# Performance work log

Hardware: AMD Instinct MI355X
Metric: run time of the kernel (lower is better)

Reference implementation:

```python
import jax, jax.numpy as jnp
import numpy as np

FORGET_BIAS = 1.0  # TF BasicLSTMCell default

def _lstm_layer(x_seq, state, W, b):
    """x_seq: [B,T,D_in]; state: [B,2*mem] = concat([c,h],1) (state_is_tuple=False).
    Returns (outputs [B,T,mem], final_state [B,2*mem])."""
    mem = state.shape[1] // 2
    c0, h0 = state[:, :mem], state[:, mem:]
    xs = jnp.swapaxes(x_seq, 0, 1)  # [T,B,D_in]

    def step(carry, x_t):
        c, h = carry
        z = jnp.concatenate([x_t, h], axis=-1) @ W + b  # [B,4*mem]
        i, j, f, o = jnp.split(z, 4, axis=-1)           # TF gate order i,j,f,o
        c = c * jax.nn.sigmoid(f + FORGET_BIAS) + jax.nn.sigmoid(i) * jnp.tanh(j)
        h = jnp.tanh(c) * jax.nn.sigmoid(o)
        return (c, h), h

    (c, h), hs = jax.lax.scan(step, (c0, h0), xs)
    return jnp.swapaxes(hs, 0, 1), jnp.concatenate([c, h], axis=-1)


def setup_inputs() -> dict:
    key = jax.random.key(0)
    ks = jax.random.split(key, 4)
    B, T, V, MEM = 64, 512, 256, 1024
    s = lambda n: 1.0 / np.sqrt(n)
    return {
        "x": jax.random.normal(ks[0], (B, T, V), jnp.float32),
        "state0": jnp.zeros((B, 2 * MEM), jnp.float32),
        "state1": jnp.zeros((B, 2 * MEM), jnp.float32),
        "W0": jax.random.normal(ks[1], (V + MEM, 4 * MEM), jnp.float32) * s(V + MEM),
        "b0": jnp.zeros((4 * MEM,), jnp.float32),
        "W1": jax.random.normal(ks[2], (2 * MEM, 4 * MEM), jnp.float32) * s(2 * MEM),
        "b1": jnp.zeros((4 * MEM,), jnp.float32),
        "W_out": jax.random.normal(ks[3], (MEM, V), jnp.float32) * s(MEM),
        "b_out": jnp.zeros((V,), jnp.float32),
    }


def reference(x, state0, state1, W0, b0, W1, b1, W_out, b_out):
    h0_seq, fs0 = _lstm_layer(x, state0, W0, b0)
    h1_seq, fs1 = _lstm_layer(h0_seq, state1, W1, b1)
    outputs = h1_seq @ W_out + b_out  # dense projection to out_vector_size
    final_state = jnp.stack([fs0, fs1], axis=0)  # [n_layers, B, 2*mem]
    return outputs, final_state
```

## Files before the change

kernel.cpp:

```cpp
#include <hip/hip_runtime.h>
#include <stdint.h>

typedef __bf16 bf16;
typedef __attribute__((ext_vector_type(8))) __bf16 bf16x8;
typedef __attribute__((ext_vector_type(4))) float f32x4;
typedef __attribute__((ext_vector_type(4))) unsigned u32x4;

#define OFF_W0P   0ull
#define SZ_W0P    10485760ull
#define OFF_W1P   (OFF_W0P + SZ_W0P)
#define SZ_W1P    16777216ull
#define OFF_WOUT  (OFF_W1P + SZ_W1P)
#define SZ_WOUT   524288ull
#define OFF_B0P   (OFF_WOUT + SZ_WOUT)
#define OFF_B1P   (OFF_B0P + 16384ull)
#define OFF_BOP   (OFF_B1P + 16384ull)
#define OFF_BAR   (OFF_BOP + 1024ull)
#define OFF_FLAG  (OFF_BAR + 128ull)
#define OFF_H0PP  (OFF_BAR + 256ull)
#define OFF_H1PP  (OFF_H0PP + 262144ull)
#define OFF_XP    (OFF_H1PP + 262144ull)
#define SZ_XP     16777216ull
#define OFF_FLAGS (OFF_XP + SZ_XP)
#define OFF_REL   (OFF_FLAGS + 1024ull)

#define OUT_FS0   8388608
#define OUT_FS1   8519680

#define LDS_PARTP 106496
#define LDS_TOTAL 110592

#define CPOL_CC 17

typedef const __attribute__((address_space(1))) void gvoid_t;
typedef __attribute__((address_space(3))) void lvoid_t;

__device__ __forceinline__ void gl_lds16(void* lds, const void* g) {
  __builtin_amdgcn_global_load_lds((gvoid_t*)g, (lvoid_t*)lds, 16, 0, 0);
}

__device__ __forceinline__ __amdgpu_buffer_rsrc_t make_rsrc(const void* p) {
  return __builtin_amdgcn_make_buffer_rsrc(const_cast<void*>(p), (short)0, 0xFFFFFFFFu, 0x00020000u);
}

__device__ __forceinline__ void st_h2(__amdgpu_buffer_rsrc_t rs, unsigned off, float h) {
  bf16 b = (bf16)h;
  __builtin_amdgcn_raw_buffer_store_b16(__builtin_bit_cast(unsigned short, b), rs, off, 0, CPOL_CC);
}

__device__ __forceinline__ size_t hpack_off(int b, int u) {
  return (size_t)((((b >> 4) * 32 + (u >> 5)) * 64 + ((b & 15) | (((u >> 3) & 3) << 4))) * 16 + ((u & 7) << 1));
}

__device__ __forceinline__ float sigm(float v) { return 1.0f / (1.0f + __expf(-v)); }
__device__ __forceinline__ float tanh_(float v) { return 2.0f / (1.0f + __expf(-2.0f * v)) - 1.0f; }
__device__ __forceinline__ float scrub(float v, float lim) { return fminf(fmaxf(v, -lim), lim); }

__device__ __forceinline__ float ldel(const void* p, size_t i, int fl) {
  return fl ? ((const float*)p)[i] : (float)((const bf16*)p)[i];
}

__global__ __launch_bounds__(256) void detect_kernel(const void* __restrict__ W0, char* __restrict__ ws) {
  __shared__ int cnt;
  if (threadIdx.x == 0) cnt = 0;
  __syncthreads();
  int local = 0;
  const unsigned* w = (const unsigned*)W0;
#pragma unroll
  for (int i = 0; i < 4; ++i) {
    unsigned e = (w[threadIdx.x * 4 + i] >> 7) & 0xFF;
    local += (e >= 0x68 && e <= 0x7E) ? 1 : 0;
  }
  atomicAdd(&cnt, local);
  __syncthreads();
  if (threadIdx.x == 0) *(unsigned*)(ws + OFF_FLAG) = (cnt < 512) ? 1u : 0u;
}

__global__ __launch_bounds__(256) void prep_pack(const void* __restrict__ x, const void* __restrict__ W0,
                                                 const void* __restrict__ b0, const void* __restrict__ W1,
                                                 const void* __restrict__ b1, const void* __restrict__ Wout,
                                                 const void* __restrict__ bout, char* __restrict__ ws) {
  const int fl = *(const unsigned*)(ws + OFF_FLAG);
  int id = blockIdx.x * 256 + threadIdx.x;
  if (id < 5242880) {
    int tile = id / 20480, rem = id % 20480;
    int kt = rem >> 9, l = (rem >> 3) & 63, jj = rem & 7;
    int k = kt * 32 + ((l >> 4) << 3) + jj;
    int pc = tile * 16 + (l & 15);
    ((bf16*)(ws + OFF_W0P))[id] = (bf16)ldel(W0, (size_t)k * 4096 + (pc & 3) * 1024 + (pc >> 2), fl);
  } else if (id < 13631488) {
    int id2 = id - 5242880;
    int tile = id2 >> 15, rem = id2 & 32767;
    int kt = rem >> 9, l = (rem >> 3) & 63, jj = rem & 7;
    int k = kt * 32 + ((l >> 4) << 3) + jj;
    int pc = tile * 16 + (l & 15);
    ((bf16*)(ws + OFF_W1P))[id2] = (bf16)ldel(W1, (size_t)k * 4096 + (pc & 3) * 1024 + (pc >> 2), fl);
  } else if (id < 13893632) {
    int id2 = id - 13631488;
    int kt = id2 / 8192, rem = id2 % 8192;
    int nt = rem >> 9, l = (rem >> 3) & 63, jj = rem & 7;
    ((bf16*)(ws + OFF_WOUT))[id2] = (bf16)ldel(Wout, (size_t)(kt * 32 + ((l >> 4) << 3) + jj) * 256 + nt * 16 + (l & 15), fl);
  } else if (id < 13897728) {
    int pc = id - 13893632;
    ((float*)(ws + OFF_B0P))[pc] = ldel(b0, (pc & 3) * 1024 + (pc >> 2), fl);
  } else if (id < 13901824) {
    int pc = id - 13897728;
    ((float*)(ws + OFF_B1P))[pc] = ldel(b1, (pc & 3) * 1024 + (pc >> 2), fl);
  } else if (id < 13902080) {
    int pc = id - 13901824;
    ((float*)(ws + OFF_BOP))[pc] = ldel(bout, pc, fl);
  } else if (id < 22290688) {
    int id2 = id - 13902080;
    int t = id2 >> 14, rem = id2 & 16383;
    int mt = rem >> 12, rem2 = rem & 4095;
    int kt = rem2 >> 9, l = (rem2 >> 3) & 63, j = rem2 & 7;
    int b = mt * 16 + (l & 15);
    int v = kt * 32 + ((l >> 4) << 3) + j;
    ((bf16*)(ws + OFF_XP))[id2] = (bf16)ldel(x, ((size_t)b * 512 + t) * 256 + v, fl);
  }
}

__global__ __launch_bounds__(256) void init_state(const void* __restrict__ s0, const void* __restrict__ s1,
                                                  char* __restrict__ ws) {
  const int fl = *(const unsigned*)(ws + OFF_FLAG);
  int id = blockIdx.x * 256 + threadIdx.x;
  if (id < 65536) {
    int b = id >> 10, u = id & 1023;
    *(bf16*)(ws + OFF_H0PP + 131072 + hpack_off(b, u)) = (bf16)ldel(s0, b * 2048 + 1024 + u, fl);
  } else if (id < 131072) {
    int id2 = id - 65536; int b = id2 >> 10, u = id2 & 1023;
    *(bf16*)(ws + OFF_H1PP + hpack_off(b, u)) = (bf16)ldel(s1, b * 2048 + 1024 + u, fl);
  } else if (id < 131330) {
    ((unsigned*)(ws + OFF_FLAGS))[id - 131072] = 0u;
  }
}

__global__ __launch_bounds__(256, 1) void recur_kernel(const void* __restrict__ s0, const void* __restrict__ s1,
                                                       char* __restrict__ ws, void* __restrict__ outv) {
  extern __shared__ char smem[];
  const int fl = *(const unsigned*)(ws + OFF_FLAG);
  const int tid = threadIdx.x;
  const int lane = tid & 63;
  const int wid = tid >> 6;
  const int cu = blockIdx.x;
  const int nt = cu & 15, mo = (cu >> 4) & 3, dg = cu >> 6;

  auto store_out = [&](size_t idx, float v) {
    if (fl) ((float*)outv)[idx] = v; else ((bf16*)outv)[idx] = (bf16)v;
  };

  {
    const char* g0 = ws + OFF_W0P + (size_t)cu * 40960;
    for (int off = tid * 16; off < 40960; off += 4096) gl_lds16(smem + off, g0 + off);
    const char* g1 = ws + OFF_W1P + (size_t)cu * 65536;
    for (int off = tid * 16; off < 65536; off += 4096) gl_lds16(smem + 40960 + off, g1 + off);
  }
  bf16x8 wreg[8];
#pragma unroll
  for (int i = 0; i < 8; ++i)
    wreg[i] = *(const bf16x8*)(ws + OFF_WOUT + (size_t)(((wid * 8 + i) * 16 + nt) * 64 + lane) * 16);

  const float bini0 = ((const float*)(ws + OFF_B0P))[cu * 16 + (lane & 15)];
  const float bini1 = ((const float*)(ws + OFF_B1P))[cu * 16 + (lane & 15)];
  const float boN = ((const float*)(ws + OFF_BOP))[nt * 16 + (lane & 15)];
  const int u0 = cu * 4 + ((lane & 15) >> 2);
  float c0reg[4], c1reg[4];
#pragma unroll
  for (int r = 0; r < 4; ++r) {
    int b = wid * 16 + ((lane >> 4) << 2) + r;
    c0reg[r] = ldel(s0, b * 2048 + u0, fl);
    c1reg[r] = ldel(s1, b * 2048 + u0, fl);
  }

  const __amdgpu_buffer_rsrc_t rs = make_rsrc(ws);
  unsigned* flags = (unsigned*)(ws + OFF_FLAGS);
  unsigned* rel   = (unsigned*)(ws + OFF_REL);
  const char* dummy = ws + (size_t)lane * 16;
  const char* lb0 = smem + (size_t)lane * 16;
  const char* lb1 = smem + 40960 + (size_t)lane * 16;

  __syncthreads();

  bf16x8 pf0, pf1, pf2, pf3, pf4, pf5, pf6, pf7;
  f32x4 accP;

  for (int it = 0; it < 517; ++it) {
    const bool a0 = (it < 512);
    const bool a1 = (it >= 1 && it <= 512);
    const bool last = (it == 516);
    const int p = (it - 2 - dg) & 3;
    const int tP = it - 2 - p;
    const bool pw = (it >= 2 && tP >= 0 && tP <= 511);
    const char* h0src = ws + OFF_H0PP + (size_t)((it + 1) & 1) * 131072;
    const char* h1src = ws + OFF_H1PP + (size_t)((it + 1) & 1) * 131072;

    const char* ph0 = (it <= 512) ? (h0src + (size_t)(wid * 32) * 1024 + (size_t)lane * 16) : dummy;
    const char* ph1 = a1 ? (h1src + (size_t)(wid * 32) * 1024 + (size_t)lane * 16) : dummy;

    if (pw && p == 0) {
      const char* pm = h1src + (size_t)(mo * 32 + wid * 8) * 1024 + (size_t)lane * 16;
      pf0 = *(const bf16x8*)(pm);
      pf1 = *(const bf16x8*)(pm + 1024);
      pf2 = *(const bf16x8*)(pm + 2048);
      pf3 = *(const bf16x8*)(pm + 3072);
      pf4 = *(const bf16x8*)(pm + 4096);
      pf5 = *(const bf16x8*)(pm + 5120);
      pf6 = *(const bf16x8*)(pm + 6144);
      pf7 = *(const bf16x8*)(pm + 7168);
#pragma unroll
      for (int r = 0; r < 4; ++r) accP[r] = 0.f;
    }

    f32x4 acc0, acc1;
#pragma unroll
    for (int r = 0; r < 4; ++r) { acc0[r] = bini0; acc1[r] = bini1; }

    if (it < 514) {
      const char* px = a0 ? (ws + OFF_XP + (size_t)((it * 4 + wid) * 8) * 1024 + (size_t)lane * 16) : dummy;

      bf16x8 ring[24];
#pragma unroll
      for (int s = 0; s < 24; ++s)
        ring[s] = *(const bf16x8*)(s < 8 ? px + s * 1024 : ph0 + (s - 8) * 1024);
#pragma unroll
      for (int s = 0; s < 72; ++s) {
        bf16x8 af = ring[s % 24];
        const int f = s + 24;
        if (f < 72)
          ring[s % 24] = *(const bf16x8*)(f < 40 ? ph0 + (f - 8) * 1024 : ph1 + (f - 40) * 1024);
        if (s < 40)
          acc0 = __builtin_amdgcn_mfma_f32_16x16x32_bf16(af, *(const bf16x8*)(lb0 + s * 1024), acc0, 0, 0, 0);
        if (s >= 8)
          acc1 = __builtin_amdgcn_mfma_f32_16x16x32_bf16(af, *(const bf16x8*)(lb1 + (s - 8) * 1024), acc1, 0, 0, 0);
      }
    }

    if (pw) {
      switch (p) {
        case 0:
          accP = __builtin_amdgcn_mfma_f32_16x16x32_bf16(pf0, wreg[0], accP, 0, 0, 0);
          accP = __builtin_amdgcn_mfma_f32_16x16x32_bf16(pf1, wreg[1], accP, 0, 0, 0);
          break;
        case 1:
          accP = __builtin_amdgcn_mfma_f32_16x16x32_bf16(pf2, wreg[2], accP, 0, 0, 0);
          accP = __builtin_amdgcn_mfma_f32_16x16x32_bf16(pf3, wreg[3], accP, 0, 0, 0);
          break;
        case 2:
          accP = __builtin_amdgcn_mfma_f32_16x16x32_bf16(pf4, wreg[4], accP, 0, 0, 0);
          accP = __builtin_amdgcn_mfma_f32_16x16x32_bf16(pf5, wreg[5], accP, 0, 0, 0);
          break;
        default:
          accP = __builtin_amdgcn_mfma_f32_16x16x32_bf16(pf6, wreg[6], accP, 0, 0, 0);
          accP = __builtin_amdgcn_mfma_f32_16x16x32_bf16(pf7, wreg[7], accP, 0, 0, 0);
          break;
      }
    }

    const int base = lane & 60;
    if (a0) {
      const unsigned h0w = (unsigned)(OFF_H0PP) + (unsigned)(it & 1) * 131072u;
#pragma unroll
      for (int r = 0; r < 4; ++r) {
        float z = acc0[r];
        float zi = scrub(__shfl(z, base + 0, 64), 80.f);
        float zj = scrub(__shfl(z, base + 1, 64), 80.f);
        float zf = scrub(__shfl(z, base + 2, 64), 80.f);
        float zo = scrub(__shfl(z, base + 3, 64), 80.f);
        float c = c0reg[r];
        c = c * sigm(zf + 1.0f) + sigm(zi) * tanh_(zj);
        c = scrub(c, 1000.f);
        float h = tanh_(c) * sigm(zo);
        c0reg[r] = c;
        if ((lane & 3) == 0) {
          int b = wid * 16 + ((lane >> 4) << 2) + r;
          st_h2(rs, h0w + (unsigned)hpack_off(b, u0), h);
          if (it == 511) { store_out(OUT_FS0 + b * 2048 + u0, c); store_out(OUT_FS0 + b * 2048 + 1024 + u0, h); }
        }
      }
    }
    if (a1) {
      const unsigned h1w = (unsigned)(OFF_H1PP) + (unsigned)(it & 1) * 131072u;
#pragma unroll
      for (int r = 0; r < 4; ++r) {
        float z = acc1[r];
        float zi = scrub(__shfl(z, base + 0, 64), 80.f);
        float zj = scrub(__shfl(z, base + 1, 64), 80.f);
        float zf = scrub(__shfl(z, base + 2, 64), 80.f);
        float zo = scrub(__shfl(z, base + 3, 64), 80.f);
        float c = c1reg[r];
        c = c * sigm(zf + 1.0f) + sigm(zi) * tanh_(zj);
        c = scrub(c, 1000.f);
        float h = tanh_(c) * sigm(zo);
        c1reg[r] = c;
        if ((lane & 3) == 0) {
          int b = wid * 16 + ((lane >> 4) << 2) + r;
          st_h2(rs, h1w + (unsigned)hpack_off(b, u0), h);
          if (it == 512) { store_out(OUT_FS1 + b * 2048 + u0, c); store_out(OUT_FS1 + b * 2048 + 1024 + u0, h); }
        }
      }
    }
    if (pw && p == 3) {
      *(f32x4*)(smem + LDS_PARTP + (size_t)(wid * 64 + lane) * 16) = accP;
      __syncthreads();
      if (wid == 0) {
        f32x4 sm = *(const f32x4*)(smem + LDS_PARTP + (size_t)lane * 16);
#pragma unroll
        for (int w = 1; w < 4; ++w) {
          f32x4 q = *(const f32x4*)(smem + LDS_PARTP + (size_t)(w * 64 + lane) * 16);
#pragma unroll
          for (int r = 0; r < 4; ++r) sm[r] += q[r];
        }
#pragma unroll
        for (int r = 0; r < 4; ++r) {
          int b = mo * 16 + ((lane >> 4) << 2) + r;
          store_out(((size_t)b * 512 + tP) * 256 + nt * 16 + (lane & 15), sm[r] + boN);
        }
      }
    }
    if (last) break;

    asm volatile("s_waitcnt vmcnt(0)" ::: "memory");
    __syncthreads();
    if (tid == 0)
      __hip_atomic_store(flags + cu, (unsigned)(it + 1), __ATOMIC_RELAXED, __HIP_MEMORY_SCOPE_AGENT);
    if (cu == 0) {
      while (__hip_atomic_load(flags + tid, __ATOMIC_RELAXED, __HIP_MEMORY_SCOPE_AGENT) < (unsigned)(it + 1))
        __builtin_amdgcn_s_sleep(8);
      __syncthreads();
      if (tid == 0)
        __hip_atomic_store(rel, (unsigned)(it + 1), __ATOMIC_RELAXED, __HIP_MEMORY_SCOPE_AGENT);
    }
    if (tid == 0) {
      while (__hip_atomic_load(rel, __ATOMIC_RELAXED, __HIP_MEMORY_SCOPE_AGENT) < (unsigned)(it + 1))
        __builtin_amdgcn_s_sleep(8);
      __builtin_amdgcn_fence(__ATOMIC_ACQUIRE, "agent");
    }
    __syncthreads();
  }
}

extern "C" void kernel_launch(void* const* d_in, const int* in_sizes, int n_in,
                              void* d_out, int out_size, void* d_ws, size_t ws_size,
                              hipStream_t stream) {
  const void* x    = d_in[0];
  const void* s0   = d_in[1];
  const void* s1   = d_in[2];
  const void* W0   = d_in[3];
  const void* b0   = d_in[4];
  const void* W1   = d_in[5];
  const void* b1   = d_in[6];
  const void* Wout = d_in[7];
  const void* bout = d_in[8];
  char* ws = (char*)d_ws;
  (void)in_sizes; (void)n_in; (void)out_size; (void)ws_size;

  hipFuncSetAttribute((const void*)recur_kernel, hipFuncAttributeMaxDynamicSharedMemorySize, LDS_TOTAL);

  hipLaunchKernelGGL(detect_kernel, dim3(1),     dim3(256), 0, stream, W0, ws);
  hipLaunchKernelGGL(prep_pack,     dim3(87073), dim3(256), 0, stream, x, W0, b0, W1, b1, Wout, bout, ws);
  hipLaunchKernelGGL(init_state,    dim3(514),   dim3(256), 0, stream, s0, s1, ws);
  hipLaunchKernelGGL(recur_kernel,  dim3(256),   dim3(256), LDS_TOTAL, stream, s0, s1, ws, d_out);
}
```

Baseline: 4.805 ms.

## Precompute next step's input-projection MFMAs during the grid barrier wait

The x-part of the layer-0 gate GEMM (8 MFMAs over the input features) does not depend on the recurrent state. It is now computed for step it+1 after the CU signals its barrier flag and before it spins on the release, so that work overlaps barrier latency. The critical-path ring loop then only streams h0/h1, which shortens the per-step dependent chain. In exchange the accumulator is carried across iterations, raising register pressure, and global x loads now sit inside the barrier window.

```diff
diff --git a/kernel.cpp b/kernel.cpp
--- a/kernel.cpp
+++ b/kernel.cpp
@@ -184,6 +184,19 @@
   bf16x8 pf0, pf1, pf2, pf3, pf4, pf5, pf6, pf7;
   f32x4 accP;
 
+  f32x4 acc0n;
+  {
+    const char* px0 = ws + OFF_XP + (size_t)(wid * 8) * 1024 + (size_t)lane * 16;
+    bf16x8 xr[8];
+#pragma unroll
+    for (int s = 0; s < 8; ++s) xr[s] = *(const bf16x8*)(px0 + s * 1024);
+#pragma unroll
+    for (int r = 0; r < 4; ++r) acc0n[r] = bini0;
+#pragma unroll
+    for (int s = 0; s < 8; ++s)
+      acc0n = __builtin_amdgcn_mfma_f32_16x16x32_bf16(xr[s], *(const bf16x8*)(lb0 + s * 1024), acc0n, 0, 0, 0);
+  }
+
   for (int it = 0; it < 517; ++it) {
     const bool a0 = (it < 512);
     const bool a1 = (it >= 1 && it <= 512);
@@ -211,27 +224,24 @@
       for (int r = 0; r < 4; ++r) accP[r] = 0.f;
     }
 
-    f32x4 acc0, acc1;
-#pragma unroll
-    for (int r = 0; r < 4; ++r) { acc0[r] = bini0; acc1[r] = bini1; }
+    f32x4 acc0 = acc0n, acc1;
+#pragma unroll
+    for (int r = 0; r < 4; ++r) acc1[r] = bini1;
 
     if (it < 514) {
-      const char* px = a0 ? (ws + OFF_XP + (size_t)((it * 4 + wid) * 8) * 1024 + (size_t)lane * 16) : dummy;
-
       bf16x8 ring[24];
 #pragma unroll
       for (int s = 0; s < 24; ++s)
-        ring[s] = *(const bf16x8*)(s < 8 ? px + s * 1024 : ph0 + (s - 8) * 1024);
-#pragma unroll
-      for (int s = 0; s < 72; ++s) {
-        bf16x8 af = ring[s % 24];
+        ring[s] = *(const bf16x8*)(ph0 + s * 1024);
+#pragma unroll
+      for (int s = 8; s < 72; ++s) {
+        bf16x8 af = ring[(s - 8) % 24];
         const int f = s + 24;
         if (f < 72)
-          ring[s % 24] = *(const bf16x8*)(f < 40 ? ph0 + (f - 8) * 1024 : ph1 + (f - 40) * 1024);
+          ring[(s - 8) % 24] = *(const bf16x8*)(f < 40 ? ph0 + (f - 8) * 1024 : ph1 + (f - 40) * 1024);
         if (s < 40)
           acc0 = __builtin_amdgcn_mfma_f32_16x16x32_bf16(af, *(const bf16x8*)(lb0 + s * 1024), acc0, 0, 0, 0);
-        if (s >= 8)
-          acc1 = __builtin_amdgcn_mfma_f32_16x16x32_bf16(af, *(const bf16x8*)(lb1 + (s - 8) * 1024), acc1, 0, 0, 0);
+        acc1 = __builtin_amdgcn_mfma_f32_16x16x32_bf16(af, *(const bf16x8*)(lb1 + (s - 8) * 1024), acc1, 0, 0, 0);
       }
     }
 
@@ -323,6 +333,20 @@
     __syncthreads();
     if (tid == 0)
       __hip_atomic_store(flags + cu, (unsigned)(it + 1), __ATOMIC_RELAXED, __HIP_MEMORY_SCOPE_AGENT);
+
+    {
+      const char* pxn = (it + 1 < 512)
+          ? (ws + OFF_XP + (size_t)(((it + 1) * 4 + wid) * 8) * 1024 + (size_t)lane * 16) : dummy;
+      bf16x8 xr[8];
+#pragma unroll
+      for (int s = 0; s < 8; ++s) xr[s] = *(const bf16x8*)(pxn + s * 1024);
+#pragma unroll
+      for (int r = 0; r < 4; ++r) acc0n[r] = bini0;
+#pragma unroll
+      for (int s = 0; s < 8; ++s)
+        acc0n = __builtin_amdgcn_mfma_f32_16x16x32_bf16(xr[s], *(const bf16x8*)(lb0 + s * 1024), acc0n, 0, 0, 0);
+    }
+
     if (cu == 0) {
       while (__hip_atomic_load(flags + tid, __ATOMIC_RELAXED, __HIP_MEMORY_SCOPE_AGENT) < (unsigned)(it + 1))
         __builtin_amdgcn_s_sleep(8);
```

Result: slower. 5.872 ms (+22.2%).
